# Performance work log

Hardware: AMD Instinct MI355X
Metric: run time of the kernel (lower is better)

## Reference

```python
import jax, jax.numpy as jnp
import numpy as np

N, NFEAT, NHID, NCLASS, NLAYERS = 10000, 512, 256, 40, 8
LAMDA, ALPHA = 0.5, 0.1
EDGE_P = 0.003  # avg degree ~30


def setup_inputs() -> dict:
    key = jax.random.key(0)
    ks = jax.random.split(key, 8)
    x = jax.random.normal(ks[0], (N, NFEAT), dtype=jnp.float32)
    # binary adjacency with zero diagonal (normalize_adj asserts diag==0)
    adj = (jax.random.uniform(ks[1], (N, N)) < EDGE_P).astype(jnp.float32)
    adj = adj * (1.0 - jnp.eye(N, dtype=jnp.float32))
    # GraphConvolution.reset_parameters: uniform(-1/sqrt(out), 1/sqrt(out))
    s = 1.0 / np.sqrt(NHID)
    conv_w = jax.random.uniform(ks[2], (NLAYERS, NHID, NHID), jnp.float32, -s, s)
    s0 = 1.0 / np.sqrt(NFEAT)
    w0 = jax.random.uniform(ks[3], (NFEAT, NHID), jnp.float32, -s0, s0)
    b0 = jax.random.uniform(ks[4], (NHID,), jnp.float32, -s0, s0)
    s1 = 1.0 / np.sqrt(NHID)
    w1 = jax.random.uniform(ks[5], (NHID, NCLASS), jnp.float32, -s1, s1)
    b1 = jax.random.uniform(ks[6], (NCLASS,), jnp.float32, -s1, s1)
    return {"x": x, "adj": adj, "w0": w0, "b0": b0, "conv_w": conv_w, "w1": w1, "b1": b1}


def reference(x, adj, w0, b0, conv_w, w1, b1):
    n = adj.shape[0]
    # normalize_adj: A_hat = A + I; D^{-1/2} A_hat D^{-1/2}
    a_hat = adj + jnp.eye(n, dtype=adj.dtype)
    d_inv_sqrt = jax.lax.rsqrt(jnp.sum(a_hat, axis=1))
    a_norm = a_hat * d_inv_sqrt[:, None] * d_inv_sqrt[None, :]

    # dropout is a no-op in eval mode
    h0 = jax.nn.relu(x @ w0 + b0)  # [N, NHID]
    thetas = jnp.log(LAMDA / jnp.arange(1, NLAYERS + 1, dtype=jnp.float32) + 1.0)

    def step(h, wt):
        w, theta = wt
        hi = a_norm @ h                              # aggregation
        support = (1.0 - ALPHA) * hi + ALPHA * h0    # initial-residual mix (variant=False: r = support)
        out = theta * (support @ w) + (1.0 - theta) * support
        return jax.nn.relu(out), None

    h, _ = jax.lax.scan(step, h0, (conv_w, thetas))
    logits = h @ w1 + b1  # [N, NCLASS]
    return jax.nn.log_softmax(logits, axis=1)
```

## Files before the change

### kernel.cpp

```cpp
#include <hip/hip_runtime.h>
#include <math.h>

#define NN 10000
#define NFEAT 512
#define NHID 256
#define NCLASS 40
#define NLAYERS 8
#define MAXDEG 96

typedef __attribute__((ext_vector_type(8))) short bf16x8;
typedef __attribute__((ext_vector_type(4))) float floatx4;
typedef __attribute__((ext_vector_type(2))) float floatx2;
typedef __attribute__((ext_vector_type(4))) unsigned short ushort4v;

__device__ __forceinline__ unsigned short f2bf(float f) {
    union { float f; unsigned int u; } v; v.f = f;
    unsigned int r = v.u + 0x7fffu + ((v.u >> 16) & 1u);
    return (unsigned short)(r >> 16);
}
__device__ __forceinline__ float bf2f(unsigned short h) {
    union { unsigned int u; float f; } v; v.u = ((unsigned int)h) << 16;
    return v.f;
}
__device__ __forceinline__ unsigned char f2fp8(float f) {
    return (unsigned char)(__builtin_amdgcn_cvt_pk_fp8_f32(f, f, 0, false) & 0xFF);
}

__global__ __launch_bounds__(256) void build_graph(const float* __restrict__ adj,
                                                   int* __restrict__ cnt,
                                                   int* __restrict__ ell,
                                                   float* __restrict__ dinv) {
    int i = blockIdx.x;
    __shared__ int scnt;
    if (threadIdx.x == 0) scnt = 0;
    __syncthreads();
    const float4* row = (const float4*)(adj + (size_t)i * NN);
    const int nv = NN / 4;
    int* erow = ell + (size_t)i * MAXDEG;
    for (int f = threadIdx.x; f < nv; f += 256) {
        float4 v = row[f];
        if (v.x != 0.0f) { int s = atomicAdd(&scnt, 1); if (s < MAXDEG) erow[s] = 4*f + 0; }
        if (v.y != 0.0f) { int s = atomicAdd(&scnt, 1); if (s < MAXDEG) erow[s] = 4*f + 1; }
        if (v.z != 0.0f) { int s = atomicAdd(&scnt, 1); if (s < MAXDEG) erow[s] = 4*f + 2; }
        if (v.w != 0.0f) { int s = atomicAdd(&scnt, 1); if (s < MAXDEG) erow[s] = 4*f + 3; }
    }
    __syncthreads();
    if (threadIdx.x == 0) {
        int c = scnt;
        cnt[i] = (c < MAXDEG) ? c : MAXDEG;
        dinv[i] = rsqrtf(1.0f + (float)c);
    }
}

__global__ __launch_bounds__(256) void prep_ell(int* __restrict__ ell,
                                                const int* __restrict__ cnt,
                                                const float* __restrict__ dinv,
                                                float* __restrict__ scl_g) {
    int idx = blockIdx.x * 256 + threadIdx.x;
    if (idx >= NN * MAXDEG) return;
    int i = idx / MAXDEG, e = idx % MAXDEG;
    if (e < cnt[i]) {
        scl_g[idx] = dinv[ell[idx]];
    } else {
        scl_g[idx] = 0.0f;
        ell[idx] = 0;
    }
}

__global__ __launch_bounds__(256) void convert_x(const float* __restrict__ x,
                                                 unsigned short* __restrict__ xb) {
    int idx = blockIdx.x * 256 + threadIdx.x;
    float4 v = ((const float4*)x)[idx];
    ushort4v o;
    o.x = f2bf(v.x); o.y = f2bf(v.y); o.z = f2bf(v.z); o.w = f2bf(v.w);
    ((ushort4v*)xb)[idx] = o;
}

__global__ __launch_bounds__(256) void convert_h8(const unsigned short* __restrict__ hb,
                                                  unsigned int* __restrict__ h8) {
    int idx = blockIdx.x * 256 + threadIdx.x;
    ushort4v v = ((const ushort4v*)hb)[idx];
    unsigned int p = __builtin_amdgcn_cvt_pk_fp8_f32(bf2f(v.x), bf2f(v.y), 0, false);
    p = __builtin_amdgcn_cvt_pk_fp8_f32(bf2f(v.z), bf2f(v.w), p, true);
    h8[idx] = p;
}

__global__ __launch_bounds__(256) void prep_weights(const float* __restrict__ w0,
                                                    const float* __restrict__ cw,
                                                    unsigned short* __restrict__ w0t,
                                                    unsigned short* __restrict__ Mt) {
    int idx = blockIdx.x * 256 + threadIdx.x;
    if (idx < 131072) {
        int n = idx >> 9, k = idx & 511;
        w0t[idx] = f2bf(w0[(size_t)k * 256 + n]);
    } else {
        int j = idx - 131072;
        int l = j >> 16;
        int r = j & 65535;
        int n = r >> 8, k = r & 255;
        float theta = logf(0.5f / (float)(l + 1) + 1.0f);
        float v = theta * cw[(size_t)l * 65536 + (size_t)k * 256 + n];
        if (k == n) v += 1.0f - theta;
        Mt[j] = f2bf(v);
    }
}

__global__ __launch_bounds__(512, 4) void gemm0_mfma(const unsigned short* __restrict__ xb,
                                                     const unsigned short* __restrict__ w0t,
                                                     const float* __restrict__ b0,
                                                     unsigned short* __restrict__ h0b) {
    int t = threadIdx.x, wv = t >> 6, lane = t & 63;
    int lrow = lane & 15, quad = lane >> 4;
    int r0 = blockIdx.x * 16;

    bf16x8 a[16];
    const unsigned short* arow = xb + (size_t)(r0 + lrow) * NFEAT + quad * 8;
    #pragma unroll
    for (int f = 0; f < 16; ++f)
        a[f] = *(const bf16x8*)(arow + f * 32);

    #pragma unroll 1
    for (int n = 0; n < 2; ++n) {
        int nt = wv * 2 + n;
        floatx4 acc = {0.f, 0.f, 0.f, 0.f};
        const unsigned short* wrow = w0t + (size_t)(nt * 16 + lrow) * NFEAT + quad * 8;
        #pragma unroll
        for (int f = 0; f < 16; ++f) {
            bf16x8 b = *(const bf16x8*)(wrow + f * 32);
            acc = __builtin_amdgcn_mfma_f32_16x16x32_bf16(a[f], b, acc, 0, 0, 0);
        }
        int col = nt * 16 + lrow;
        float bias = b0[col];
        #pragma unroll
        for (int r = 0; r < 4; ++r) {
            int row = r0 + quad * 4 + r;
            h0b[(size_t)row * NHID + col] = f2bf(fmaxf(acc[r] + bias, 0.f));
        }
    }
}

template<bool LAST>
__global__ __launch_bounds__(512, 6) void layer_fused(const unsigned int* __restrict__ h8,
                                                      const unsigned short* __restrict__ h0b,
                                                      const float* __restrict__ dinv,
                                                      const int* __restrict__ cnt,
                                                      const int* __restrict__ ell,
                                                      const float* __restrict__ scl_g,
                                                      const unsigned short* __restrict__ Mt,
                                                      const float* __restrict__ w1,
                                                      const float* __restrict__ b1,
                                                      unsigned char* __restrict__ h8_out,
                                                      float* __restrict__ out) {
    __shared__ unsigned short supb[16][264];
    __shared__ float hs[LAST ? 16 * 264 : 4];

    int t = threadIdx.x;
    int wv = __builtin_amdgcn_readfirstlane(t >> 6);
    int lane = t & 63;
    int r0 = blockIdx.x * 16;

    #pragma unroll 1
    for (int rr = 0; rr < 2; ++rr) {
        int lr = wv * 2 + rr;
        int i  = r0 + lr;
        int deg8 = (cnt[i] + 7) & ~7;
        float di = dinv[i];
        const int*   ellrow = ell   + (size_t)i * MAXDEG;
        const float* sclrow = scl_g + (size_t)i * MAXDEG;
        unsigned int su = h8[(size_t)i * 64 + lane];
        floatx2 slo = __builtin_amdgcn_cvt_pk_f32_fp8(su, false);
        floatx2 shi = __builtin_amdgcn_cvt_pk_f32_fp8(su, true);
        float4 acc;
        acc.x = di * slo.x;
        acc.y = di * slo.y;
        acc.z = di * shi.x;
        acc.w = di * shi.y;
        #pragma unroll 1
        for (int e0 = 0; e0 < deg8; e0 += 8) {
            #pragma unroll
            for (int u = 0; u < 8; ++u) {
                int   j = ellrow[e0 + u];
                float s = sclrow[e0 + u];
                unsigned int xu = h8[(size_t)j * 64 + lane];
                floatx2 lo = __builtin_amdgcn_cvt_pk_f32_fp8(xu, false);
                floatx2 hi = __builtin_amdgcn_cvt_pk_f32_fp8(xu, true);
                acc.x = fmaf(s, lo.x, acc.x);
                acc.y = fmaf(s, lo.y, acc.y);
                acc.z = fmaf(s, hi.x, acc.z);
                acc.w = fmaf(s, hi.y, acc.w);
            }
        }
        ushort4v h0v = ((const ushort4v*)h0b)[(size_t)i * 64 + lane];
        ushort4v ob;
        ob.x = f2bf(0.9f * (di * acc.x) + 0.1f * bf2f(h0v.x));
        ob.y = f2bf(0.9f * (di * acc.y) + 0.1f * bf2f(h0v.y));
        ob.z = f2bf(0.9f * (di * acc.z) + 0.1f * bf2f(h0v.z));
        ob.w = f2bf(0.9f * (di * acc.w) + 0.1f * bf2f(h0v.w));
        *(ushort4v*)&supb[lr][4 * lane] = ob;
    }
    __syncthreads();

    int lrow = lane & 15, quad = lane >> 4;
    bf16x8 a[8];
    #pragma unroll
    for (int f = 0; f < 8; ++f)
        a[f] = *(const bf16x8*)&supb[lrow][quad * 8 + f * 32];

    #pragma unroll 1
    for (int n = 0; n < 2; ++n) {
        int nt = wv * 2 + n;
        floatx4 acc = {0.f, 0.f, 0.f, 0.f};
        const unsigned short* wrow = Mt + (size_t)(nt * 16 + lrow) * NHID + quad * 8;
        #pragma unroll
        for (int f = 0; f < 8; ++f) {
            bf16x8 b = *(const bf16x8*)(wrow + f * 32);
            acc = __builtin_amdgcn_mfma_f32_16x16x32_bf16(a[f], b, acc, 0, 0, 0);
        }
        int col = nt * 16 + lrow;
        #pragma unroll
        for (int r = 0; r < 4; ++r) {
            int lr2 = quad * 4 + r;
            float o = fmaxf(acc[r], 0.f);
            if (LAST) {
                hs[lr2 * 264 + col] = o;
            } else {
                h8_out[(size_t)(r0 + lr2) * NHID + col] = f2fp8(o);
            }
        }
    }

    if (LAST) {
        __syncthreads();
        #pragma unroll 1
        for (int rr = 0; rr < 2; ++rr) {
            int lr = wv * 2 + rr;
            const float* hr = hs + lr * 264;
            float logit = -1e30f;
            if (lane < NCLASS) {
                float acc = b1[lane];
                #pragma unroll 8
                for (int k = 0; k < NHID; ++k)
                    acc = fmaf(hr[k], w1[k * NCLASS + lane], acc);
                logit = acc;
            }
            float m = logit;
            #pragma unroll
            for (int off = 32; off > 0; off >>= 1)
                m = fmaxf(m, __shfl_xor(m, off, 64));
            float e = (lane < NCLASS) ? expf(logit - m) : 0.0f;
            float ssum = e;
            #pragma unroll
            for (int off = 32; off > 0; off >>= 1)
                ssum += __shfl_xor(ssum, off, 64);
            float lse = m + logf(ssum);
            if (lane < NCLASS)
                out[(size_t)(r0 + lr) * NCLASS + lane] = logit - lse;
        }
    }
}

extern "C" void kernel_launch(void* const* d_in, const int* in_sizes, int n_in,
                              void* d_out, int out_size, void* d_ws, size_t ws_size,
                              hipStream_t stream) {
    const float* x      = (const float*)d_in[0];
    const float* adj    = (const float*)d_in[1];
    const float* w0     = (const float*)d_in[2];
    const float* b0     = (const float*)d_in[3];
    const float* conv_w = (const float*)d_in[4];
    const float* w1     = (const float*)d_in[5];
    const float* b1     = (const float*)d_in[6];
    float* out = (float*)d_out;

    char* ws = (char*)d_ws;
    size_t off = 0;
    auto alloc = [&](size_t bytes) -> void* {
        void* p = ws + off;
        off = (off + bytes + 255) & ~(size_t)255;
        return p;
    };
    float*          dinv  = (float*)alloc((size_t)NN * 4);
    int*            cnt   = (int*)  alloc((size_t)NN * 4);
    int*            ell   = (int*)  alloc((size_t)NN * MAXDEG * 4);
    float*          scl_g = (float*)alloc((size_t)NN * MAXDEG * 4);
    unsigned short* xb    = (unsigned short*)alloc((size_t)NN * NFEAT * 2);
    unsigned short* w0t   = (unsigned short*)alloc((size_t)NFEAT * NHID * 2);
    unsigned short* Mt    = (unsigned short*)alloc((size_t)NLAYERS * NHID * NHID * 2);
    unsigned short* h0b   = (unsigned short*)alloc((size_t)NN * NHID * 2);
    unsigned int*   h08   = (unsigned int*)alloc((size_t)NN * NHID);
    unsigned int*   hP8   = (unsigned int*)alloc((size_t)NN * NHID);
    unsigned int*   hQ8   = (unsigned int*)alloc((size_t)NN * NHID);

    build_graph<<<NN, 256, 0, stream>>>(adj, cnt, ell, dinv);
    convert_x<<<(NN * NFEAT / 4) / 256, 256, 0, stream>>>(x, xb);
    prep_weights<<<(131072 + NLAYERS * NHID * NHID) / 256, 256, 0, stream>>>(w0, conv_w, w0t, Mt);
    prep_ell<<<(NN * MAXDEG + 255) / 256, 256, 0, stream>>>(ell, cnt, dinv, scl_g);

    gemm0_mfma<<<NN / 16, 512, 0, stream>>>(xb, w0t, b0, h0b);
    convert_h8<<<(NN * NHID / 4) / 256, 256, 0, stream>>>(h0b, h08);

    const unsigned int* hc8 = h08;
    for (int l = 0; l < NLAYERS; ++l) {
        unsigned int* nxt = (l & 1) ? hQ8 : hP8;
        const unsigned short* wt = Mt + (size_t)l * NHID * NHID;
        if (l == NLAYERS - 1)
            layer_fused<true><<<NN / 16, 512, 0, stream>>>(hc8, h0b, dinv, cnt, ell, scl_g, wt, w1, b1, nullptr, out);
        else
            layer_fused<false><<<NN / 16, 512, 0, stream>>>(hc8, h0b, dinv, cnt, ell, scl_g, wt, nullptr, nullptr, (unsigned char*)nxt, nullptr);
        hc8 = nxt;
    }
}
```

Measured before the change: 780.7 us.

## Fuse GCN layers into one persistent kernel with grid barriers

Replaces the eight per-layer launches with a single persistent kernel of 625 blocks that synchronises between layers using an atomic counter grid barrier. Each block caches its ELL neighbour indices and scales in shared memory once, so the prep_ell pass and the scl_g array are no longer needed. The bf16 conversion of x is folded into gemm0, and gemm0 now also writes the fp8 copy of h0, removing the convert_x and convert_h8 kernels. The grid barrier assumes all 625 blocks are co-resident, with a timeout break as a fallback; if they are not co-resident, correctness and progress are at risk.

```diff
diff --git a/kernel.cpp b/kernel.cpp
--- a/kernel.cpp
+++ b/kernel.cpp
@@ -7,6 +7,7 @@
 #define NCLASS 40
 #define NLAYERS 8
 #define MAXDEG 96
+#define GRID_L 625
 
 typedef __attribute__((ext_vector_type(8))) short bf16x8;
 typedef __attribute__((ext_vector_type(4))) float floatx4;
@@ -52,39 +53,6 @@
     }
 }
 
-__global__ __launch_bounds__(256) void prep_ell(int* __restrict__ ell,
-                                                const int* __restrict__ cnt,
-                                                const float* __restrict__ dinv,
-                                                float* __restrict__ scl_g) {
-    int idx = blockIdx.x * 256 + threadIdx.x;
-    if (idx >= NN * MAXDEG) return;
-    int i = idx / MAXDEG, e = idx % MAXDEG;
-    if (e < cnt[i]) {
-        scl_g[idx] = dinv[ell[idx]];
-    } else {
-        scl_g[idx] = 0.0f;
-        ell[idx] = 0;
-    }
-}
-
-__global__ __launch_bounds__(256) void convert_x(const float* __restrict__ x,
-                                                 unsigned short* __restrict__ xb) {
-    int idx = blockIdx.x * 256 + threadIdx.x;
-    float4 v = ((const float4*)x)[idx];
-    ushort4v o;
-    o.x = f2bf(v.x); o.y = f2bf(v.y); o.z = f2bf(v.z); o.w = f2bf(v.w);
-    ((ushort4v*)xb)[idx] = o;
-}
-
-__global__ __launch_bounds__(256) void convert_h8(const unsigned short* __restrict__ hb,
-                                                  unsigned int* __restrict__ h8) {
-    int idx = blockIdx.x * 256 + threadIdx.x;
-    ushort4v v = ((const ushort4v*)hb)[idx];
-    unsigned int p = __builtin_amdgcn_cvt_pk_fp8_f32(bf2f(v.x), bf2f(v.y), 0, false);
-    p = __builtin_amdgcn_cvt_pk_fp8_f32(bf2f(v.z), bf2f(v.w), p, true);
-    h8[idx] = p;
-}
-
 __global__ __launch_bounds__(256) void prep_weights(const float* __restrict__ w0,
                                                     const float* __restrict__ cw,
                                                     unsigned short* __restrict__ w0t,
@@ -105,19 +73,28 @@
     }
 }
 
-__global__ __launch_bounds__(512, 4) void gemm0_mfma(const unsigned short* __restrict__ xb,
+__global__ __launch_bounds__(512, 4) void gemm0_mfma(const float* __restrict__ x,
                                                      const unsigned short* __restrict__ w0t,
                                                      const float* __restrict__ b0,
-                                                     unsigned short* __restrict__ h0b) {
+                                                     unsigned short* __restrict__ h0b,
+                                                     unsigned char* __restrict__ h08) {
     int t = threadIdx.x, wv = t >> 6, lane = t & 63;
     int lrow = lane & 15, quad = lane >> 4;
     int r0 = blockIdx.x * 16;
 
     bf16x8 a[16];
-    const unsigned short* arow = xb + (size_t)(r0 + lrow) * NFEAT + quad * 8;
+    const float4* xr = (const float4*)(x + (size_t)(r0 + lrow) * NFEAT) + quad * 2;
     #pragma unroll
-    for (int f = 0; f < 16; ++f)
-        a[f] = *(const bf16x8*)(arow + f * 32);
+    for (int f = 0; f < 16; ++f) {
+        float4 lo = xr[f * 8];
+        float4 hi = xr[f * 8 + 1];
+        bf16x8 av;
+        av[0] = (short)f2bf(lo.x); av[1] = (short)f2bf(lo.y);
+        av[2] = (short)f2bf(lo.z); av[3] = (short)f2bf(lo.w);
+        av[4] = (short)f2bf(hi.x); av[5] = (short)f2bf(hi.y);
+        av[6] = (short)f2bf(hi.z); av[7] = (short)f2bf(hi.w);
+        a[f] = av;
+    }
 
     #pragma unroll 1
     for (int n = 0; n < 2; ++n) {
@@ -134,128 +111,173 @@
         #pragma unroll
         for (int r = 0; r < 4; ++r) {
             int row = r0 + quad * 4 + r;
-            h0b[(size_t)row * NHID + col] = f2bf(fmaxf(acc[r] + bias, 0.f));
-        }
-    }
-}
-
-template<bool LAST>
-__global__ __launch_bounds__(512, 6) void layer_fused(const unsigned int* __restrict__ h8,
-                                                      const unsigned short* __restrict__ h0b,
-                                                      const float* __restrict__ dinv,
-                                                      const int* __restrict__ cnt,
-                                                      const int* __restrict__ ell,
-                                                      const float* __restrict__ scl_g,
-                                                      const unsigned short* __restrict__ Mt,
-                                                      const float* __restrict__ w1,
-                                                      const float* __restrict__ b1,
-                                                      unsigned char* __restrict__ h8_out,
-                                                      float* __restrict__ out) {
+            float o = fmaxf(acc[r] + bias, 0.f);
+            h0b[(size_t)row * NHID + col] = f2bf(o);
+            h08[(size_t)row * NHID + col] = f2fp8(o);
+        }
+    }
+}
+
+__global__ __launch_bounds__(512, 6) void gcn_layers(
+        const unsigned int* __restrict__ h08,
+        unsigned int* __restrict__ hP8,
+        unsigned int* __restrict__ hQ8,
+        const unsigned short* __restrict__ h0b,
+        const float* __restrict__ dinv,
+        const int* __restrict__ cnt,
+        const int* __restrict__ ell,
+        const unsigned short* __restrict__ Mt,
+        const float* __restrict__ w1,
+        const float* __restrict__ b1,
+        float* __restrict__ out,
+        int* __restrict__ barrier) {
+    __shared__ int            sj[16][MAXDEG];
+    __shared__ float          scl[16][MAXDEG];
     __shared__ unsigned short supb[16][264];
-    __shared__ float hs[LAST ? 16 * 264 : 4];
+    __shared__ float          hs[16 * 264];
+    __shared__ int            sdeg[16];
+    __shared__ float          sdinv[16];
 
     int t = threadIdx.x;
-    int wv = __builtin_amdgcn_readfirstlane(t >> 6);
+    int wv = t >> 6;
     int lane = t & 63;
     int r0 = blockIdx.x * 16;
 
+    for (int idx = t; idx < 16 * MAXDEG; idx += 512) {
+        int lr = idx / MAXDEG, e = idx % MAXDEG;
+        int i = r0 + lr;
+        int d = cnt[i];
+        int j = 0; float s = 0.0f;
+        if (e < d) { j = ell[(size_t)i * MAXDEG + e]; s = dinv[j]; }
+        sj[lr][e] = j;
+        scl[lr][e] = s;
+    }
+    if (t < 16) {
+        int i = r0 + t;
+        sdeg[t] = (cnt[i] + 7) & ~7;
+        sdinv[t] = dinv[i];
+    }
+    __syncthreads();
+
+    const unsigned int* cur = h08;
+    int lrow = lane & 15, quad = lane >> 4;
+
+    #pragma unroll 1
+    for (int l = 0; l < NLAYERS; ++l) {
+        #pragma unroll 1
+        for (int rr = 0; rr < 2; ++rr) {
+            int lr = wv * 2 + rr;
+            int i  = r0 + lr;
+            int deg8 = sdeg[lr];
+            float di = sdinv[lr];
+            unsigned int su = cur[(size_t)i * 64 + lane];
+            floatx2 slo = __builtin_amdgcn_cvt_pk_f32_fp8(su, false);
+            floatx2 shi = __builtin_amdgcn_cvt_pk_f32_fp8(su, true);
+            float4 acc;
+            acc.x = di * slo.x;
+            acc.y = di * slo.y;
+            acc.z = di * shi.x;
+            acc.w = di * shi.y;
+            #pragma unroll 1
+            for (int e0 = 0; e0 < deg8; e0 += 8) {
+                #pragma unroll
+                for (int u = 0; u < 8; ++u) {
+                    int   j = sj[lr][e0 + u];
+                    float s = scl[lr][e0 + u];
+                    unsigned int xu = cur[(size_t)j * 64 + lane];
+                    floatx2 lo = __builtin_amdgcn_cvt_pk_f32_fp8(xu, false);
+                    floatx2 hi = __builtin_amdgcn_cvt_pk_f32_fp8(xu, true);
+                    acc.x = fmaf(s, lo.x, acc.x);
+                    acc.y = fmaf(s, lo.y, acc.y);
+                    acc.z = fmaf(s, hi.x, acc.z);
+                    acc.w = fmaf(s, hi.y, acc.w);
+                }
+            }
+            ushort4v h0v = ((const ushort4v*)h0b)[(size_t)i * 64 + lane];
+            ushort4v ob;
+            ob.x = f2bf(0.9f * (di * acc.x) + 0.1f * bf2f(h0v.x));
+            ob.y = f2bf(0.9f * (di * acc.y) + 0.1f * bf2f(h0v.y));
+            ob.z = f2bf(0.9f * (di * acc.z) + 0.1f * bf2f(h0v.z));
+            ob.w = f2bf(0.9f * (di * acc.w) + 0.1f * bf2f(h0v.w));
+            *(ushort4v*)&supb[lr][4 * lane] = ob;
+        }
+        __syncthreads();
+
+        bf16x8 a[8];
+        #pragma unroll
+        for (int f = 0; f < 8; ++f)
+            a[f] = *(const bf16x8*)&supb[lrow][quad * 8 + f * 32];
+
+        unsigned int* nxt = (l & 1) ? hQ8 : hP8;
+        unsigned char* nxtb = (unsigned char*)nxt;
+        const unsigned short* Ml = Mt + (size_t)l * NHID * NHID;
+        #pragma unroll 1
+        for (int n = 0; n < 2; ++n) {
+            int nt = wv * 2 + n;
+            floatx4 acc = {0.f, 0.f, 0.f, 0.f};
+            const unsigned short* wrow = Ml + (size_t)(nt * 16 + lrow) * NHID + quad * 8;
+            #pragma unroll
+            for (int f = 0; f < 8; ++f) {
+                bf16x8 b = *(const bf16x8*)(wrow + f * 32);
+                acc = __builtin_amdgcn_mfma_f32_16x16x32_bf16(a[f], b, acc, 0, 0, 0);
+            }
+            int col = nt * 16 + lrow;
+            #pragma unroll
+            for (int r = 0; r < 4; ++r) {
+                int lr2 = quad * 4 + r;
+                float o = fmaxf(acc[r], 0.f);
+                if (l == NLAYERS - 1) {
+                    hs[lr2 * 264 + col] = o;
+                } else {
+                    nxtb[(size_t)(r0 + lr2) * NHID + col] = f2fp8(o);
+                }
+            }
+        }
+
+        if (l < NLAYERS - 1) {
+            __syncthreads();
+            if (t == 0) {
+                __threadfence();
+                __hip_atomic_fetch_add(&barrier[l], 1, __ATOMIC_RELEASE,
+                                       __HIP_MEMORY_SCOPE_AGENT);
+                int it = 0;
+                while (__hip_atomic_load(&barrier[l], __ATOMIC_RELAXED,
+                                         __HIP_MEMORY_SCOPE_AGENT) < GRID_L) {
+                    __builtin_amdgcn_s_sleep(4);
+                    if (++it > (1 << 24)) break;
+                }
+                __threadfence();
+            }
+            __syncthreads();
+            cur = nxt;
+        }
+    }
+
+    __syncthreads();
     #pragma unroll 1
     for (int rr = 0; rr < 2; ++rr) {
         int lr = wv * 2 + rr;
-        int i  = r0 + lr;
-        int deg8 = (cnt[i] + 7) & ~7;
-        float di = dinv[i];
-        const int*   ellrow = ell   + (size_t)i * MAXDEG;
-        const float* sclrow = scl_g + (size_t)i * MAXDEG;
-        unsigned int su = h8[(size_t)i * 64 + lane];
-        floatx2 slo = __builtin_amdgcn_cvt_pk_f32_fp8(su, false);
-        floatx2 shi = __builtin_amdgcn_cvt_pk_f32_fp8(su, true);
-        float4 acc;
-        acc.x = di * slo.x;
-        acc.y = di * slo.y;
-        acc.z = di * shi.x;
-        acc.w = di * shi.y;
-        #pragma unroll 1
-        for (int e0 = 0; e0 < deg8; e0 += 8) {
-            #pragma unroll
-            for (int u = 0; u < 8; ++u) {
-                int   j = ellrow[e0 + u];
-                float s = sclrow[e0 + u];
-                unsigned int xu = h8[(size_t)j * 64 + lane];
-                floatx2 lo = __builtin_amdgcn_cvt_pk_f32_fp8(xu, false);
-                floatx2 hi = __builtin_amdgcn_cvt_pk_f32_fp8(xu, true);
-                acc.x = fmaf(s, lo.x, acc.x);
-                acc.y = fmaf(s, lo.y, acc.y);
-                acc.z = fmaf(s, hi.x, acc.z);
-                acc.w = fmaf(s, hi.y, acc.w);
-            }
-        }
-        ushort4v h0v = ((const ushort4v*)h0b)[(size_t)i * 64 + lane];
-        ushort4v ob;
-        ob.x = f2bf(0.9f * (di * acc.x) + 0.1f * bf2f(h0v.x));
-        ob.y = f2bf(0.9f * (di * acc.y) + 0.1f * bf2f(h0v.y));
-        ob.z = f2bf(0.9f * (di * acc.z) + 0.1f * bf2f(h0v.z));
-        ob.w = f2bf(0.9f * (di * acc.w) + 0.1f * bf2f(h0v.w));
-        *(ushort4v*)&supb[lr][4 * lane] = ob;
-    }
-    __syncthreads();
-
-    int lrow = lane & 15, quad = lane >> 4;
-    bf16x8 a[8];
-    #pragma unroll
-    for (int f = 0; f < 8; ++f)
-        a[f] = *(const bf16x8*)&supb[lrow][quad * 8 + f * 32];
-
-    #pragma unroll 1
-    for (int n = 0; n < 2; ++n) {
-        int nt = wv * 2 + n;
-        floatx4 acc = {0.f, 0.f, 0.f, 0.f};
-        const unsigned short* wrow = Mt + (size_t)(nt * 16 + lrow) * NHID + quad * 8;
-        #pragma unroll
-        for (int f = 0; f < 8; ++f) {
-            bf16x8 b = *(const bf16x8*)(wrow + f * 32);
-            acc = __builtin_amdgcn_mfma_f32_16x16x32_bf16(a[f], b, acc, 0, 0, 0);
-        }
-        int col = nt * 16 + lrow;
-        #pragma unroll
-        for (int r = 0; r < 4; ++r) {
-            int lr2 = quad * 4 + r;
-            float o = fmaxf(acc[r], 0.f);
-            if (LAST) {
-                hs[lr2 * 264 + col] = o;
-            } else {
-                h8_out[(size_t)(r0 + lr2) * NHID + col] = f2fp8(o);
-            }
-        }
-    }
-
-    if (LAST) {
-        __syncthreads();
-        #pragma unroll 1
-        for (int rr = 0; rr < 2; ++rr) {
-            int lr = wv * 2 + rr;
-            const float* hr = hs + lr * 264;
-            float logit = -1e30f;
-            if (lane < NCLASS) {
-                float acc = b1[lane];
-                #pragma unroll 8
-                for (int k = 0; k < NHID; ++k)
-                    acc = fmaf(hr[k], w1[k * NCLASS + lane], acc);
-                logit = acc;
-            }
-            float m = logit;
-            #pragma unroll
-            for (int off = 32; off > 0; off >>= 1)
-                m = fmaxf(m, __shfl_xor(m, off, 64));
-            float e = (lane < NCLASS) ? expf(logit - m) : 0.0f;
-            float ssum = e;
-            #pragma unroll
-            for (int off = 32; off > 0; off >>= 1)
-                ssum += __shfl_xor(ssum, off, 64);
-            float lse = m + logf(ssum);
-            if (lane < NCLASS)
-                out[(size_t)(r0 + lr) * NCLASS + lane] = logit - lse;
-        }
+        const float* hr = hs + lr * 264;
+        float logit = -1e30f;
+        if (lane < NCLASS) {
+            float acc = b1[lane];
+            #pragma unroll 8
+            for (int k = 0; k < NHID; ++k)
+                acc = fmaf(hr[k], w1[k * NCLASS + lane], acc);
+            logit = acc;
+        }
+        float m = logit;
+        #pragma unroll
+        for (int off = 32; off > 0; off >>= 1)
+            m = fmaxf(m, __shfl_xor(m, off, 64));
+        float e = (lane < NCLASS) ? expf(logit - m) : 0.0f;
+        float ssum = e;
+        #pragma unroll
+        for (int off = 32; off > 0; off >>= 1)
+            ssum += __shfl_xor(ssum, off, 64);
+        float lse = m + logf(ssum);
+        if (lane < NCLASS)
+            out[(size_t)(r0 + lr) * NCLASS + lane] = logit - lse;
     }
 }
 
@@ -281,31 +303,20 @@
     float*          dinv  = (float*)alloc((size_t)NN * 4);
     int*            cnt   = (int*)  alloc((size_t)NN * 4);
     int*            ell   = (int*)  alloc((size_t)NN * MAXDEG * 4);
-    float*          scl_g = (float*)alloc((size_t)NN * MAXDEG * 4);
-    unsigned short* xb    = (unsigned short*)alloc((size_t)NN * NFEAT * 2);
     unsigned short* w0t   = (unsigned short*)alloc((size_t)NFEAT * NHID * 2);
     unsigned short* Mt    = (unsigned short*)alloc((size_t)NLAYERS * NHID * NHID * 2);
     unsigned short* h0b   = (unsigned short*)alloc((size_t)NN * NHID * 2);
     unsigned int*   h08   = (unsigned int*)alloc((size_t)NN * NHID);
     unsigned int*   hP8   = (unsigned int*)alloc((size_t)NN * NHID);
     unsigned int*   hQ8   = (unsigned int*)alloc((size_t)NN * NHID);
+    int*            barrier = (int*)alloc(64 * 4);
+
+    hipMemsetAsync(barrier, 0, 64 * 4, stream);
 
     build_graph<<<NN, 256, 0, stream>>>(adj, cnt, ell, dinv);
-    convert_x<<<(NN * NFEAT / 4) / 256, 256, 0, stream>>>(x, xb);
     prep_weights<<<(131072 + NLAYERS * NHID * NHID) / 256, 256, 0, stream>>>(w0, conv_w, w0t, Mt);
-    prep_ell<<<(NN * MAXDEG + 255) / 256, 256, 0, stream>>>(ell, cnt, dinv, scl_g);
-
-    gemm0_mfma<<<NN / 16, 512, 0, stream>>>(xb, w0t, b0, h0b);
-    convert_h8<<<(NN * NHID / 4) / 256, 256, 0, stream>>>(h0b, h08);
-
-    const unsigned int* hc8 = h08;
-    for (int l = 0; l < NLAYERS; ++l) {
-        unsigned int* nxt = (l & 1) ? hQ8 : hP8;
-        const unsigned short* wt = Mt + (size_t)l * NHID * NHID;
-        if (l == NLAYERS - 1)
-            layer_fused<true><<<NN / 16, 512, 0, stream>>>(hc8, h0b, dinv, cnt, ell, scl_g, wt, w1, b1, nullptr, out);
-        else
-            layer_fused<false><<<NN / 16, 512, 0, stream>>>(hc8, h0b, dinv, cnt, ell, scl_g, wt, nullptr, nullptr, (unsigned char*)nxt, nullptr);
-        hc8 = nxt;
-    }
-}
+    gemm0_mfma<<<NN / 16, 512, 0, stream>>>(x, w0t, b0, h0b, (unsigned char*)h08);
+
+    gcn_layers<<<GRID_L, 512, 0, stream>>>(h08, hP8, hQ8, h0b, dinv, cnt, ell,
+                                           Mt, w1, b1, out, barrier);
+}
```

Result: slower. 1.476 ms (+89.1%).

## Fuse input conversions into gemm0 and interleave two-row SpMM gathers

Applied to the files above, without the earlier changes.

The x-to-bf16 conversion is folded into the first GEMM's A-fragment loads, and the fp8 copy of h0 is written directly from the GEMM epilogue. This removes two separate conversion kernels and their intermediate buffers. The aggregation loop in each layer now processes a wave's two rows together, issuing both rows' neighbour gathers in the same iteration to raise memory-level parallelism. The two-row loop runs to the larger of the two degrees, so some padded ELL entries get extra loads, and more registers are live.

```diff
diff --git a/kernel.cpp b/kernel.cpp
--- a/kernel.cpp
+++ b/kernel.cpp
@@ -67,24 +67,6 @@
     }
 }
 
-__global__ __launch_bounds__(256) void convert_x(const float* __restrict__ x,
-                                                 unsigned short* __restrict__ xb) {
-    int idx = blockIdx.x * 256 + threadIdx.x;
-    float4 v = ((const float4*)x)[idx];
-    ushort4v o;
-    o.x = f2bf(v.x); o.y = f2bf(v.y); o.z = f2bf(v.z); o.w = f2bf(v.w);
-    ((ushort4v*)xb)[idx] = o;
-}
-
-__global__ __launch_bounds__(256) void convert_h8(const unsigned short* __restrict__ hb,
-                                                  unsigned int* __restrict__ h8) {
-    int idx = blockIdx.x * 256 + threadIdx.x;
-    ushort4v v = ((const ushort4v*)hb)[idx];
-    unsigned int p = __builtin_amdgcn_cvt_pk_fp8_f32(bf2f(v.x), bf2f(v.y), 0, false);
-    p = __builtin_amdgcn_cvt_pk_fp8_f32(bf2f(v.z), bf2f(v.w), p, true);
-    h8[idx] = p;
-}
-
 __global__ __launch_bounds__(256) void prep_weights(const float* __restrict__ w0,
                                                     const float* __restrict__ cw,
                                                     unsigned short* __restrict__ w0t,
@@ -105,19 +87,28 @@
     }
 }
 
-__global__ __launch_bounds__(512, 4) void gemm0_mfma(const unsigned short* __restrict__ xb,
+__global__ __launch_bounds__(512, 4) void gemm0_mfma(const float* __restrict__ x,
                                                      const unsigned short* __restrict__ w0t,
                                                      const float* __restrict__ b0,
-                                                     unsigned short* __restrict__ h0b) {
+                                                     unsigned short* __restrict__ h0b,
+                                                     unsigned char* __restrict__ h08) {
     int t = threadIdx.x, wv = t >> 6, lane = t & 63;
     int lrow = lane & 15, quad = lane >> 4;
     int r0 = blockIdx.x * 16;
 
     bf16x8 a[16];
-    const unsigned short* arow = xb + (size_t)(r0 + lrow) * NFEAT + quad * 8;
+    const float4* xr = (const float4*)(x + (size_t)(r0 + lrow) * NFEAT) + quad * 2;
     #pragma unroll
-    for (int f = 0; f < 16; ++f)
-        a[f] = *(const bf16x8*)(arow + f * 32);
+    for (int f = 0; f < 16; ++f) {
+        float4 lo = xr[f * 8];
+        float4 hi = xr[f * 8 + 1];
+        bf16x8 av;
+        av[0] = (short)f2bf(lo.x); av[1] = (short)f2bf(lo.y);
+        av[2] = (short)f2bf(lo.z); av[3] = (short)f2bf(lo.w);
+        av[4] = (short)f2bf(hi.x); av[5] = (short)f2bf(hi.y);
+        av[6] = (short)f2bf(hi.z); av[7] = (short)f2bf(hi.w);
+        a[f] = av;
+    }
 
     #pragma unroll 1
     for (int n = 0; n < 2; ++n) {
@@ -134,7 +125,9 @@
         #pragma unroll
         for (int r = 0; r < 4; ++r) {
             int row = r0 + quad * 4 + r;
-            h0b[(size_t)row * NHID + col] = f2bf(fmaxf(acc[r] + bias, 0.f));
+            float o = fmaxf(acc[r] + bias, 0.f);
+            h0b[(size_t)row * NHID + col] = f2bf(o);
+            h08[(size_t)row * NHID + col] = f2fp8(o);
         }
     }
 }
@@ -159,44 +152,68 @@
     int lane = t & 63;
     int r0 = blockIdx.x * 16;
 
-    #pragma unroll 1
-    for (int rr = 0; rr < 2; ++rr) {
-        int lr = wv * 2 + rr;
-        int i  = r0 + lr;
-        int deg8 = (cnt[i] + 7) & ~7;
-        float di = dinv[i];
-        const int*   ellrow = ell   + (size_t)i * MAXDEG;
-        const float* sclrow = scl_g + (size_t)i * MAXDEG;
-        unsigned int su = h8[(size_t)i * 64 + lane];
-        floatx2 slo = __builtin_amdgcn_cvt_pk_f32_fp8(su, false);
-        floatx2 shi = __builtin_amdgcn_cvt_pk_f32_fp8(su, true);
-        float4 acc;
-        acc.x = di * slo.x;
-        acc.y = di * slo.y;
-        acc.z = di * shi.x;
-        acc.w = di * shi.y;
+    {
+        int lrA = wv * 2, lrB = wv * 2 + 1;
+        int iA = r0 + lrA, iB = r0 + lrB;
+        int degA = (cnt[iA] + 7) & ~7;
+        int degB = (cnt[iB] + 7) & ~7;
+        int maxd = degA > degB ? degA : degB;
+        float diA = dinv[iA], diB = dinv[iB];
+        const int*   ellA = ell   + (size_t)iA * MAXDEG;
+        const float* sclA = scl_g + (size_t)iA * MAXDEG;
+        const int*   ellB = ell   + (size_t)iB * MAXDEG;
+        const float* sclB = scl_g + (size_t)iB * MAXDEG;
+
+        unsigned int suA = h8[(size_t)iA * 64 + lane];
+        unsigned int suB = h8[(size_t)iB * 64 + lane];
+        floatx2 alo = __builtin_amdgcn_cvt_pk_f32_fp8(suA, false);
+        floatx2 ahi = __builtin_amdgcn_cvt_pk_f32_fp8(suA, true);
+        floatx2 blo = __builtin_amdgcn_cvt_pk_f32_fp8(suB, false);
+        floatx2 bhi = __builtin_amdgcn_cvt_pk_f32_fp8(suB, true);
+        float4 accA, accB;
+        accA.x = diA * alo.x; accA.y = diA * alo.y;
+        accA.z = diA * ahi.x; accA.w = diA * ahi.y;
+        accB.x = diB * blo.x; accB.y = diB * blo.y;
+        accB.z = diB * bhi.x; accB.w = diB * bhi.y;
+
         #pragma unroll 1
-        for (int e0 = 0; e0 < deg8; e0 += 8) {
+        for (int e0 = 0; e0 < maxd; e0 += 8) {
             #pragma unroll
             for (int u = 0; u < 8; ++u) {
-                int   j = ellrow[e0 + u];
-                float s = sclrow[e0 + u];
-                unsigned int xu = h8[(size_t)j * 64 + lane];
-                floatx2 lo = __builtin_amdgcn_cvt_pk_f32_fp8(xu, false);
-                floatx2 hi = __builtin_amdgcn_cvt_pk_f32_fp8(xu, true);
-                acc.x = fmaf(s, lo.x, acc.x);
-                acc.y = fmaf(s, lo.y, acc.y);
-                acc.z = fmaf(s, hi.x, acc.z);
-                acc.w = fmaf(s, hi.y, acc.w);
+                int   jA = ellA[e0 + u];
+                int   jB = ellB[e0 + u];
+                float sA = sclA[e0 + u];
+                float sB = sclB[e0 + u];
+                unsigned int xA = h8[(size_t)jA * 64 + lane];
+                unsigned int xB = h8[(size_t)jB * 64 + lane];
+                floatx2 lo, hi;
+                lo = __builtin_amdgcn_cvt_pk_f32_fp8(xA, false);
+                hi = __builtin_amdgcn_cvt_pk_f32_fp8(xA, true);
+                accA.x = fmaf(sA, lo.x, accA.x);
+                accA.y = fmaf(sA, lo.y, accA.y);
+                accA.z = fmaf(sA, hi.x, accA.z);
+                accA.w = fmaf(sA, hi.y, accA.w);
+                lo = __builtin_amdgcn_cvt_pk_f32_fp8(xB, false);
+                hi = __builtin_amdgcn_cvt_pk_f32_fp8(xB, true);
+                accB.x = fmaf(sB, lo.x, accB.x);
+                accB.y = fmaf(sB, lo.y, accB.y);
+                accB.z = fmaf(sB, hi.x, accB.z);
+                accB.w = fmaf(sB, hi.y, accB.w);
             }
         }
-        ushort4v h0v = ((const ushort4v*)h0b)[(size_t)i * 64 + lane];
-        ushort4v ob;
-        ob.x = f2bf(0.9f * (di * acc.x) + 0.1f * bf2f(h0v.x));
-        ob.y = f2bf(0.9f * (di * acc.y) + 0.1f * bf2f(h0v.y));
-        ob.z = f2bf(0.9f * (di * acc.z) + 0.1f * bf2f(h0v.z));
-        ob.w = f2bf(0.9f * (di * acc.w) + 0.1f * bf2f(h0v.w));
-        *(ushort4v*)&supb[lr][4 * lane] = ob;
+        ushort4v h0A = ((const ushort4v*)h0b)[(size_t)iA * 64 + lane];
+        ushort4v h0B = ((const ushort4v*)h0b)[(size_t)iB * 64 + lane];
+        ushort4v oA, oB;
+        oA.x = f2bf(0.9f * (diA * accA.x) + 0.1f * bf2f(h0A.x));
+        oA.y = f2bf(0.9f * (diA * accA.y) + 0.1f * bf2f(h0A.y));
+        oA.z = f2bf(0.9f * (diA * accA.z) + 0.1f * bf2f(h0A.z));
+        oA.w = f2bf(0.9f * (diA * accA.w) + 0.1f * bf2f(h0A.w));
+        oB.x = f2bf(0.9f * (diB * accB.x) + 0.1f * bf2f(h0B.x));
+        oB.y = f2bf(0.9f * (diB * accB.y) + 0.1f * bf2f(h0B.y));
+        oB.z = f2bf(0.9f * (diB * accB.z) + 0.1f * bf2f(h0B.z));
+        oB.w = f2bf(0.9f * (diB * accB.w) + 0.1f * bf2f(h0B.w));
+        *(ushort4v*)&supb[lrA][4 * lane] = oA;
+        *(ushort4v*)&supb[lrB][4 * lane] = oB;
     }
     __syncthreads();
 
@@ -282,7 +299,6 @@
     int*            cnt   = (int*)  alloc((size_t)NN * 4);
     int*            ell   = (int*)  alloc((size_t)NN * MAXDEG * 4);
     float*          scl_g = (float*)alloc((size_t)NN * MAXDEG * 4);
-    unsigned short* xb    = (unsigned short*)alloc((size_t)NN * NFEAT * 2);
     unsigned short* w0t   = (unsigned short*)alloc((size_t)NFEAT * NHID * 2);
     unsigned short* Mt    = (unsigned short*)alloc((size_t)NLAYERS * NHID * NHID * 2);
     unsigned short* h0b   = (unsigned short*)alloc((size_t)NN * NHID * 2);
@@ -291,12 +307,9 @@
     unsigned int*   hQ8   = (unsigned int*)alloc((size_t)NN * NHID);
 
     build_graph<<<NN, 256, 0, stream>>>(adj, cnt, ell, dinv);
-    convert_x<<<(NN * NFEAT / 4) / 256, 256, 0, stream>>>(x, xb);
     prep_weights<<<(131072 + NLAYERS * NHID * NHID) / 256, 256, 0, stream>>>(w0, conv_w, w0t, Mt);
     prep_ell<<<(NN * MAXDEG + 255) / 256, 256, 0, stream>>>(ell, cnt, dinv, scl_g);
-
-    gemm0_mfma<<<NN / 16, 512, 0, stream>>>(xb, w0t, b0, h0b);
-    convert_h8<<<(NN * NHID / 4) / 256, 256, 0, stream>>>(h0b, h08);
+    gemm0_mfma<<<NN / 16, 512, 0, stream>>>(x, w0t, b0, h0b, (unsigned char*)h08);
 
     const unsigned int* hc8 = h08;
     for (int l = 0; l < NLAYERS; ++l) {
```

After: 787.7 us. Within noise of the previous version (+0.9%).
